# Optimization experiments

Measured on AMD Instinct MI355X. Metric: run time of the kernel, lower is better.

Reference implementation:

```python
import jax, jax.numpy as jnp
import numpy as np

# Config (matches init_kwargs): num_ori=0 -> plain ConvNext path, single scale, knn-16 graph.
N, B, G, K = 16384, 8, 2048, 16   # N nodes = B graphs x G nodes, k-NN with self loops
C, BD, WF, L = 128, 128, 4, 4     # hidden, basis_dim, widening_factor, num layers
POLY_IN = 3                        # PolynomialFeatures(degree=2) on [E,1] dist -> [d, d^2, d^3]


def knn_edges(pos):
    # Graphs are contiguous blocks of G nodes (batch = node // G).
    pg = pos.reshape(B, G, 3)
    d2 = jnp.sum((pg[:, :, None, :] - pg[:, None, :, :]) ** 2, axis=-1)  # [B,G,G]
    _, idx = jax.lax.top_k(-d2, K)                                       # [B,G,K] incl. self (loop=True)
    offset = (jnp.arange(B) * G)[:, None, None]
    src = (idx + offset).reshape(-1)            # neighbor (source) node per edge, [E]
    dst = jnp.repeat(jnp.arange(B * G), K)      # center (target) node per edge, [E]
    return src, dst


def layer_norm(h, g, b):
    mu = jnp.mean(h, axis=-1, keepdims=True)
    var = jnp.var(h, axis=-1, keepdims=True)
    return (h - mu) / jnp.sqrt(var + 1e-5) * g + b


def setup_inputs() -> dict:
    key = jax.random.key(0)
    ks = jax.random.split(key, 20)
    s = 0.05
    inp = {
        'x': jax.random.normal(ks[0], (N, 65), jnp.float32),
        'pos': jax.random.normal(ks[1], (N, 3), jnp.float32),
        'batch': jnp.repeat(jnp.arange(B, dtype=jnp.int32), G),
        # x_embedder (no bias)
        'W_embed': jax.random.normal(ks[2], (65, C), jnp.float32) * s,
        # spatial basis MLP: poly(3) -> Linear -> GELU -> Linear -> GELU
        'Wb1': jax.random.normal(ks[3], (POLY_IN, BD), jnp.float32) * s,
        'bb1': jnp.zeros((BD,), jnp.float32),
        'Wb2': jax.random.normal(ks[4], (BD, BD), jnp.float32) * s,
        'bb2': jnp.zeros((BD,), jnp.float32),
        # per-layer ConvNext params (stacked over L layers)
        'Wk': jax.random.normal(ks[5], (L, BD, C), jnp.float32) * s,  # depthwise conv kernel gen
        'ln_g': jnp.ones((L, C), jnp.float32),
        'ln_b': jnp.zeros((L, C), jnp.float32),
        'W1': jax.random.normal(ks[6], (L, C, WF * C), jnp.float32) * s,
        'b1': jnp.zeros((L, WF * C), jnp.float32),
        'W2': jax.random.normal(ks[7], (L, WF * C, C), jnp.float32) * s,
        'b2': jnp.zeros((L, C), jnp.float32),
        # readout
        'Wr': jax.random.normal(ks[8], (C, 1), jnp.float32) * s,
        'br': jnp.zeros((1,), jnp.float32),
    }
    return inp


def reference(x, pos, batch, W_embed, Wb1, bb1, Wb2, bb2, Wk, ln_g, ln_b, W1, b1, W2, b2, Wr, br):
    src, dst = knn_edges(pos)
    # SEn invariant with num_ori=0: pairwise distance (eps for self-loop grad safety)
    diff = pos[src] - pos[dst]                                    # [E,3]
    d = jnp.sqrt(jnp.sum(diff * diff, axis=-1, keepdims=True) + 1e-12)  # [E,1]
    # PolynomialFeatures(degree=2): [d, d^2, d^3]
    poly = jnp.concatenate([d, d * d, d * d * d], axis=-1)        # [E,3]
    kb = jax.nn.gelu(poly @ Wb1 + bb1)
    kernel = jax.nn.gelu(kb @ Wb2 + bb2)                          # [E,BD] spatial kernel basis

    h = x @ W_embed                                               # [N,C]
    for i in range(L):
        # depthwise conv: per-edge kernel from basis, gather-multiply-scatter
        k_i = kernel @ Wk[i]                                      # [E,C]
        msg = h[src] * k_i                                        # [E,C]
        agg = jax.ops.segment_sum(msg, dst, num_segments=N)       # [N,C]
        z = layer_norm(agg, ln_g[i], ln_b[i])
        z = jax.nn.gelu(z @ W1[i] + b1[i]) @ W2[i] + b2[i]        # pointwise inverted-bottleneck
        h = h + z                                                 # residual (in==out channels)
    out = h @ Wr + br                                             # readout, [N,1] scalar output
    return out
```

## Files before the change

### kernel.cpp

```cpp
#include <hip/hip_runtime.h>
#include <hip/hip_bf16.h>

#define NN 16384
#define GG 2048
#define KNN 16
#define EE (NN*KNN)
#define NL 4

typedef _Float16 f16;
typedef _Float16 half8 __attribute__((ext_vector_type(8)));
typedef _Float16 half4 __attribute__((ext_vector_type(4)));
typedef float f32x4 __attribute__((ext_vector_type(4)));
typedef unsigned long long u64;

__device__ __forceinline__ float gelu_tanh(float x) {
  float s = x*x;
  float u = __fmaf_rn(-0.0713548194f, s, -1.5957691216f);
  float p = __expf(x*u);
  return x * __builtin_amdgcn_rcpf(1.0f + p);
}

__device__ __forceinline__ int mbcnt64(u64 m) {
  return __builtin_amdgcn_mbcnt_hi((unsigned)(m >> 32),
         __builtin_amdgcn_mbcnt_lo((unsigned)m, 0));
}

__global__ __launch_bounds__(256) void knn_kernel(const float* __restrict__ pos,
    int* __restrict__ srci, float* __restrict__ dedge) {
  __shared__ u64 sel[4][16];
  int tid = threadIdx.x;
  int wv = tid >> 6;
  int node = blockIdx.x*4 + wv;
  int lane = tid & 63;
  int base = node & ~(GG-1);
  float qx = pos[(size_t)node*3+0], qy = pos[(size_t)node*3+1], qz = pos[(size_t)node*3+2];

  float d2s[32];
  float c0 = 3.4e38f, c1 = 3.4e38f, c2 = 3.4e38f, c3 = 3.4e38f;
  #pragma unroll
  for (int it = 0; it < 32; ++it) {
    int j = it*64 + lane;
    const float* pr = pos + (size_t)(base+j)*3;
    float dx = __fsub_rn(qx, pr[0]);
    float dy = __fsub_rn(qy, pr[1]);
    float dz = __fsub_rn(qz, pr[2]);
    float d2 = __fadd_rn(__fadd_rn(__fmul_rn(dx,dx), __fmul_rn(dy,dy)), __fmul_rn(dz,dz));
    d2s[it] = d2;
    float x = d2;
    float t0 = fminf(c0, x); x = fmaxf(c0, x); c0 = t0;
    float t1 = fminf(c1, x); x = fmaxf(c1, x); c1 = t1;
    float t2 = fminf(c2, x); x = fmaxf(c2, x); c2 = t2;
    c3 = fminf(c3, x);
  }
  unsigned T = 0;
  for (int b = 30; b >= 0; --b) {
    unsigned tb = T | (1u << b);
    float tf = __uint_as_float(tb);
    int cnt = __popcll(__ballot(c0 < tf)) + __popcll(__ballot(c1 < tf))
            + __popcll(__ballot(c2 < tf)) + __popcll(__ballot(c3 < tf));
    if (cnt < 16) T = tb;
  }
  float Tf = __uint_as_float(T);
  int cless;
  if (!__any(c3 <= Tf)) {
    cless = __popcll(__ballot(c0 < Tf)) + __popcll(__ballot(c1 < Tf))
          + __popcll(__ballot(c2 < Tf)) + __popcll(__ballot(c3 < Tf));
  } else {
    T = 0;
    for (int b = 30; b >= 0; --b) {
      unsigned tb = T | (1u << b);
      float tf = __uint_as_float(tb);
      int cnt = 0;
      #pragma unroll
      for (int q = 0; q < 32; ++q) cnt += __popcll(__ballot(d2s[q] < tf));
      if (cnt < 16) T = tb;
    }
    Tf = __uint_as_float(T);
    cless = 0;
    #pragma unroll
    for (int q = 0; q < 32; ++q) cless += __popcll(__ballot(d2s[q] < Tf));
  }
  int offb = 0;
  int tieq = 16 - cless;
  #pragma unroll
  for (int it = 0; it < 32; ++it) {
    u64 mless = __ballot(d2s[it] < Tf);
    u64 mtie  = __ballot(d2s[it] == Tf);
    bool store = (d2s[it] < Tf);
    int slot = offb + mbcnt64(mless);
    offb += (int)__popcll(mless);
    if (mtie != 0 && tieq > 0) {
      int tr = mbcnt64(mtie);
      if (d2s[it] == Tf && tr < tieq) { store = true; slot = offb + tr; }
      int take = (int)__popcll(mtie); take = take < tieq ? take : tieq;
      offb += take; tieq -= take;
    }
    if (store)
      sel[wv][slot] = ((u64)__float_as_uint(d2s[it]) << 32) | (unsigned)(it*64 + lane);
  }
  if (lane < KNN) {
    u64 e = sel[wv][lane];
    int rank = 0;
    #pragma unroll
    for (int k2 = 0; k2 < 16; ++k2) rank += (sel[wv][k2] < e) ? 1 : 0;
    int j = (int)(e & 0xffffffffu);
    float d2v = __uint_as_float((unsigned)(e >> 32));
    srci[node*KNN + rank] = base + j;
    dedge[node*KNN + rank] = sqrtf(__fadd_rn(d2v, 1e-12f));
  }
}

__global__ __launch_bounds__(256) void prep_kernel(
    const float* __restrict__ Wb2, const float* __restrict__ Wk,
    const float* __restrict__ W1, const float* __restrict__ W2,
    f16* __restrict__ Wb2t, f16* __restrict__ Wkt,
    f16* __restrict__ W1t, f16* __restrict__ W2t) {
  int i = blockIdx.x*256 + threadIdx.x;
  if (i < 16384) {
    int c = i >> 7, k = i & 127;
    Wb2t[i] = (f16)Wb2[k*128 + c];
    return;
  }
  i -= 16384;
  if (i < 65536) {
    int l = i >> 14, r = i & 16383; int c = r >> 7, k = r & 127;
    Wkt[i] = (f16)Wk[l*16384 + k*128 + c];
    return;
  }
  i -= 65536;
  if (i < 262144) {
    int l = i >> 16, r = i & 65535; int c = r >> 7, k = r & 127;
    W1t[i] = (f16)W1[l*65536 + k*512 + c];
    return;
  }
  i -= 262144;
  if (i < 262144) {
    int l = i >> 16, r = i & 65535; int c = r >> 9, k = r & 511;
    W2t[i] = (f16)W2[l*65536 + k*128 + c];
  }
}

__global__ __launch_bounds__(256) void embed_kernel(const float* __restrict__ x,
    const float* __restrict__ We, float* __restrict__ h) {
  int t = threadIdx.x;
  int n = blockIdx.x*8 + (t >> 5);
  int q = (t & 31) * 4;
  f32x4 acc = {0.f,0.f,0.f,0.f};
  const float* xr = x + n*65;
  for (int k = 0; k < 65; ++k) {
    float xv = xr[k];
    f32x4 wv = *(const f32x4*)(We + k*128 + q);
    acc += xv * wv;
  }
  *(f32x4*)(h + (size_t)n*128 + q) = acc;
}

__global__ __launch_bounds__(256) void basis_kernel(const float* __restrict__ dedge,
    const float* __restrict__ Wb1, const float* __restrict__ bb1,
    const f16* __restrict__ Wb2t, const float* __restrict__ bb2,
    f16* __restrict__ kernA) {
  __shared__ f16 Wb2s[128][136];
  __shared__ f16 kb[64][136];
  int t = threadIdx.x;
  #pragma unroll
  for (int it = 0; it < 8; ++it) {
    int idx = it*256 + t;
    int row = idx >> 4, k8 = (idx & 15) * 8;
    *(half8*)&Wb2s[row][k8] = *(const half8*)&Wb2t[row*128 + k8];
  }
  __syncthreads();
  int w = t >> 6, l = t & 63;
  int row4 = l >> 4, rlo = l & 15;
  #pragma unroll
  for (int tt = 0; tt < 2; ++tt) {
    size_t Tg = (size_t)blockIdx.x*8 + (size_t)w*2 + tt;
    float d = dedge[Tg*16 + rlo];
    float d2 = d*d, d3 = d2*d;
    half8 a[4];
    #pragma unroll
    for (int kc = 0; kc < 4; ++kc) {
      int k0 = kc*32 + row4*8;
      f32x4 w1a = *(const f32x4*)&Wb1[k0],     w1b = *(const f32x4*)&Wb1[k0+4];
      f32x4 w2a = *(const f32x4*)&Wb1[128+k0], w2b = *(const f32x4*)&Wb1[128+k0+4];
      f32x4 w3a = *(const f32x4*)&Wb1[256+k0], w3b = *(const f32x4*)&Wb1[256+k0+4];
      f32x4 bba = *(const f32x4*)&bb1[k0],     bbb = *(const f32x4*)&bb1[k0+4];
      #pragma unroll
      for (int j = 0; j < 4; ++j) {
        a[kc][j]   = (f16)gelu_tanh(d*w1a[j] + d2*w2a[j] + d3*w3a[j] + bba[j]);
        a[kc][4+j] = (f16)gelu_tanh(d*w1b[j] + d2*w2b[j] + d3*w3b[j] + bbb[j]);
      }
    }
    f32x4 acc[8];
    #pragma unroll
    for (int nt = 0; nt < 8; ++nt) {
      acc[nt] = (f32x4){0.f,0.f,0.f,0.f};
      #pragma unroll
      for (int kc = 0; kc < 4; ++kc) {
        half8 b = *(const half8*)&Wb2s[nt*16 + rlo][kc*32 + row4*8];
        acc[nt] = __builtin_amdgcn_mfma_f32_16x16x32_f16(a[kc], b, acc[nt], 0, 0, 0);
      }
    }
    #pragma unroll
    for (int nt = 0; nt < 8; ++nt) {
      float bias = bb2[nt*16 + rlo];
      #pragma unroll
      for (int j = 0; j < 4; ++j)
        kb[w*16 + row4*4 + j][nt*16 + rlo] = (f16)gelu_tanh(acc[nt][j] + bias);
    }
    #pragma unroll
    for (int kc = 0; kc < 4; ++kc) {
      half8 v = *(const half8*)&kb[w*16 + rlo][kc*32 + row4*8];
      *(half8*)&kernA[((Tg*4 + kc)*64 + l)*8] = v;
    }
  }
}

#define LOADA(arr, mm) { \
  int node_ = n0 + w*4 + (mm); \
  _Pragma("unroll") \
  for (int kc = 0; kc < 4; ++kc) \
    arr[kc] = *(const half8*)&kernA[(((size_t)node_*4 + kc)*64 + l)*8]; }

#define COMPM(arr, mm) { \
  float hv[4][4]; \
  _Pragma("unroll") \
  for (int nt4 = 0; nt4 < 4; ++nt4) \
    _Pragma("unroll") \
    for (int j = 0; j < 4; ++j) \
      hv[nt4][j] = hin[(size_t)sidxA[mm][j]*128 + (hh*4 + nt4)*16 + rlo]; \
  _Pragma("unroll") \
  for (int nt4 = 0; nt4 < 4; ++nt4) { \
    f32x4 acc = {0.f,0.f,0.f,0.f}; \
    _Pragma("unroll") \
    for (int kc = 0; kc < 4; ++kc) \
      acc = __builtin_amdgcn_mfma_f32_16x16x32_f16(arr[kc], bf[nt4][kc], acc, 0, 0, 0); \
    float p = 0.f; \
    _Pragma("unroll") \
    for (int j = 0; j < 4; ++j) p += acc[j] * hv[nt4][j]; \
    p += __shfl_xor(p, 16, 64); \
    p += __shfl_xor(p, 32, 64); \
    if (l < 16) aggl[w*4 + (mm)][(hh*4 + nt4)*16 + l] = p; \
  } }

__global__ __launch_bounds__(256) void layer_kernel(const f16* __restrict__ kernA,
    const f16* __restrict__ Wkt_l, const int* __restrict__ srci,
    const float* __restrict__ hin,
    const float* __restrict__ lng, const float* __restrict__ lnb,
    const f16* __restrict__ W1t_l, const float* __restrict__ b1_l,
    const f16* __restrict__ W2t_l, const float* __restrict__ b2_l,
    float* __restrict__ hout) {
  __shared__ float aggl[16][132];
  __shared__ f16 zl[16][136];
  __shared__ f16 y1[16][520];
  int t = threadIdx.x;
  int w = t >> 6, l = t & 63;
  int row4 = l >> 4, rlo = l & 15;
  int n0 = blockIdx.x * 16;

  int sidxA[4][4];
  #pragma unroll
  for (int m = 0; m < 4; ++m)
    #pragma unroll
    for (int j = 0; j < 4; ++j)
      sidxA[m][j] = srci[(n0 + w*4 + m)*16 + row4*4 + j];

  #pragma unroll
  for (int hh = 0; hh < 2; ++hh) {
    half8 bf[4][4];
    #pragma unroll
    for (int nt4 = 0; nt4 < 4; ++nt4)
      #pragma unroll
      for (int kc = 0; kc < 4; ++kc)
        bf[nt4][kc] = *(const half8*)&Wkt_l[((hh*4 + nt4)*16 + rlo)*128 + kc*32 + row4*8];
    half8 aA[4], aB[4];
    LOADA(aA, 0)
    LOADA(aB, 1)
    COMPM(aA, 0)
    LOADA(aA, 2)
    COMPM(aB, 1)
    LOADA(aB, 3)
    COMPM(aA, 2)
    COMPM(aB, 3)
  }
  __syncthreads();
  {
    int row = w*4 + row4;
    int cb = rlo*8;
    f32x4 va = *(const f32x4*)&aggl[row][cb];
    f32x4 vb = *(const f32x4*)&aggl[row][cb+4];
    float s = va[0]+va[1]+va[2]+va[3] + vb[0]+vb[1]+vb[2]+vb[3];
    #pragma unroll
    for (int st = 1; st < 16; st <<= 1) s += __shfl_xor(s, st, 64);
    float mu = s * (1.f/128.f);
    f32x4 da = va - mu, db = vb - mu;
    float s2 = da[0]*da[0]+da[1]*da[1]+da[2]*da[2]+da[3]*da[3]
             + db[0]*db[0]+db[1]*db[1]+db[2]*db[2]+db[3]*db[3];
    #pragma unroll
    for (int st = 1; st < 16; st <<= 1) s2 += __shfl_xor(s2, st, 64);
    float inv = rsqrtf(s2*(1.f/128.f) + 1e-5f);
    f32x4 ga = *(const f32x4*)&lng[cb], gb = *(const f32x4*)&lng[cb+4];
    f32x4 ba = *(const f32x4*)&lnb[cb], bb = *(const f32x4*)&lnb[cb+4];
    f32x4 za = da*inv*ga + ba, zb = db*inv*gb + bb;
    half8 hz = { (f16)za[0],(f16)za[1],(f16)za[2],(f16)za[3],
                 (f16)zb[0],(f16)zb[1],(f16)zb[2],(f16)zb[3] };
    *(half8*)&zl[row][cb] = hz;
  }
  __syncthreads();
  half8 az[4];
  #pragma unroll
  for (int kc = 0; kc < 4; ++kc)
    az[kc] = *(const half8*)&zl[rlo][kc*32 + row4*8];
  #pragma unroll
  for (int ntl = 0; ntl < 8; ++ntl) {
    int nt = w*8 + ntl;
    int col = nt*16 + rlo;
    f32x4 acc = {0.f,0.f,0.f,0.f};
    #pragma unroll
    for (int kc = 0; kc < 4; ++kc) {
      half8 b = *(const half8*)&W1t_l[(size_t)col*128 + kc*32 + row4*8];
      acc = __builtin_amdgcn_mfma_f32_16x16x32_f16(az[kc], b, acc, 0, 0, 0);
    }
    float bias = b1_l[col];
    #pragma unroll
    for (int j = 0; j < 4; ++j)
      y1[row4*4 + j][col] = (f16)gelu_tanh(acc[j] + bias);
  }
  __syncthreads();
  half8 a2[16];
  #pragma unroll
  for (int kc2 = 0; kc2 < 16; ++kc2)
    a2[kc2] = *(const half8*)&y1[rlo][kc2*32 + row4*8];
  f32x4 acc2[2] = {{0.f,0.f,0.f,0.f},{0.f,0.f,0.f,0.f}};
  #pragma unroll
  for (int nt2 = 0; nt2 < 2; ++nt2) {
    int c = (w*2 + nt2)*16 + rlo;
    #pragma unroll
    for (int kc2 = 0; kc2 < 16; ++kc2) {
      half8 b = *(const half8*)&W2t_l[(size_t)c*512 + kc2*32 + row4*8];
      acc2[nt2] = __builtin_amdgcn_mfma_f32_16x16x32_f16(a2[kc2], b, acc2[nt2], 0, 0, 0);
    }
  }
  #pragma unroll
  for (int nt2 = 0; nt2 < 2; ++nt2) {
    int col = (w*2 + nt2)*16 + rlo;
    float bias = b2_l[col];
    #pragma unroll
    for (int j = 0; j < 4; ++j) {
      size_t n = (size_t)(n0 + row4*4 + j);
      hout[n*128 + col] = acc2[nt2][j] + bias + hin[n*128 + col];
    }
  }
}

__global__ __launch_bounds__(256) void readout_kernel(const float* __restrict__ h,
    const float* __restrict__ Wr, const float* __restrict__ br, float* __restrict__ out) {
  int n = blockIdx.x*256 + threadIdx.x;
  f32x4 acc = {0.f,0.f,0.f,0.f};
  #pragma unroll
  for (int cb = 0; cb < 32; ++cb) {
    f32x4 hv = *(const f32x4*)(h + (size_t)n*128 + cb*4);
    f32x4 wv = *(const f32x4*)(Wr + cb*4);
    acc += hv*wv;
  }
  out[n] = acc[0]+acc[1]+acc[2]+acc[3] + br[0];
}

extern "C" void kernel_launch(void* const* d_in, const int* in_sizes, int n_in,
                              void* d_out, int out_size, void* d_ws, size_t ws_size,
                              hipStream_t stream) {
  const float* x   = (const float*)d_in[0];
  const float* pos = (const float*)d_in[1];
  const float* We  = (const float*)d_in[3];
  const float* Wb1 = (const float*)d_in[4];
  const float* bb1 = (const float*)d_in[5];
  const float* Wb2 = (const float*)d_in[6];
  const float* bb2 = (const float*)d_in[7];
  const float* Wk  = (const float*)d_in[8];
  const float* lng = (const float*)d_in[9];
  const float* lnb = (const float*)d_in[10];
  const float* W1  = (const float*)d_in[11];
  const float* b1  = (const float*)d_in[12];
  const float* W2  = (const float*)d_in[13];
  const float* b2  = (const float*)d_in[14];
  const float* Wr  = (const float*)d_in[15];
  const float* br  = (const float*)d_in[16];
  float* out = (float*)d_out;

  char* p = (char*)d_ws;
  int*   srci  = (int*)p;     p += (size_t)EE*4;
  float* dedge = (float*)p;   p += (size_t)EE*4;
  f16*   kernA = (f16*)p;     p += (size_t)EE*128*2;
  float* hA    = (float*)p;   p += (size_t)NN*128*4;
  float* hB    = (float*)p;   p += (size_t)NN*128*4;
  f16* Wb2t    = (f16*)p;     p += (size_t)16384*2;
  f16* Wkt     = (f16*)p;     p += (size_t)65536*2;
  f16* W1t     = (f16*)p;     p += (size_t)262144*2;
  f16* W2t     = (f16*)p;     p += (size_t)262144*2;

  prep_kernel<<<2368, 256, 0, stream>>>(Wb2, Wk, W1, W2, Wb2t, Wkt, W1t, W2t);
  knn_kernel<<<NN/4, 256, 0, stream>>>(pos, srci, dedge);
  basis_kernel<<<2048, 256, 0, stream>>>(dedge, Wb1, bb1, Wb2t, bb2, kernA);
  embed_kernel<<<NN/8, 256, 0, stream>>>(x, We, hA);
  float* hin = hA;
  for (int lyr = 0; lyr < NL; ++lyr) {
    float* hout = (hin == hA) ? hB : hA;
    layer_kernel<<<NN/16, 256, 0, stream>>>(kernA, Wkt + lyr*16384, srci, hin,
        lng + lyr*128, lnb + lyr*128,
        W1t + (size_t)lyr*65536, b1 + lyr*512, W2t + (size_t)lyr*65536, b2 + lyr*128, hout);
    hin = hout;
  }
  readout_kernel<<<NN/256, 256, 0, stream>>>(hin, Wr, br, out);
}
```

Before: 353.9 us.

## Prefetch neighbor features, remap block order, and cap occupancy in layer kernel

Splits the gather of neighbor h values from the compute macro so each node's hin loads are issued together with its kernel-basis loads, one node ahead of the MFMA work, to hide gather latency. It also permutes block indices so consecutive blocks work on nodes spread across graphs, probably to spread L2/channel traffic, and adds a min-blocks-per-CU hint to launch_bounds. The prefetch raises register pressure. It also leaves an empty dead loop at the end of the kernel.

```diff
diff --git a/kernel.cpp b/kernel.cpp
--- a/kernel.cpp
+++ b/kernel.cpp
@@ -221,13 +221,14 @@
   for (int kc = 0; kc < 4; ++kc) \
     arr[kc] = *(const half8*)&kernA[(((size_t)node_*4 + kc)*64 + l)*8]; }
 
-#define COMPM(arr, mm) { \
-  float hv[4][4]; \
+#define PREH(hvv, mm) { \
   _Pragma("unroll") \
   for (int nt4 = 0; nt4 < 4; ++nt4) \
     _Pragma("unroll") \
     for (int j = 0; j < 4; ++j) \
-      hv[nt4][j] = hin[(size_t)sidxA[mm][j]*128 + (hh*4 + nt4)*16 + rlo]; \
+      hvv[nt4][j] = hin[(size_t)sidxA[mm][j]*128 + (hh*4 + nt4)*16 + rlo]; }
+
+#define COMPU(arr, hvv, mm) { \
   _Pragma("unroll") \
   for (int nt4 = 0; nt4 < 4; ++nt4) { \
     f32x4 acc = {0.f,0.f,0.f,0.f}; \
@@ -236,13 +237,13 @@
       acc = __builtin_amdgcn_mfma_f32_16x16x32_f16(arr[kc], bf[nt4][kc], acc, 0, 0, 0); \
     float p = 0.f; \
     _Pragma("unroll") \
-    for (int j = 0; j < 4; ++j) p += acc[j] * hv[nt4][j]; \
+    for (int j = 0; j < 4; ++j) p += acc[j] * hvv[nt4][j]; \
     p += __shfl_xor(p, 16, 64); \
     p += __shfl_xor(p, 32, 64); \
     if (l < 16) aggl[w*4 + (mm)][(hh*4 + nt4)*16 + l] = p; \
   } }
 
-__global__ __launch_bounds__(256) void layer_kernel(const f16* __restrict__ kernA,
+__global__ __launch_bounds__(256, 4) void layer_kernel(const f16* __restrict__ kernA,
     const f16* __restrict__ Wkt_l, const int* __restrict__ srci,
     const float* __restrict__ hin,
     const float* __restrict__ lng, const float* __restrict__ lnb,
@@ -255,7 +256,8 @@
   int t = threadIdx.x;
   int w = t >> 6, l = t & 63;
   int row4 = l >> 4, rlo = l & 15;
-  int n0 = blockIdx.x * 16;
+  int bid = (blockIdx.x & 7)*128 + (blockIdx.x >> 3);
+  int n0 = bid * 16;
 
   int sidxA[4][4];
   #pragma unroll
@@ -273,14 +275,15 @@
       for (int kc = 0; kc < 4; ++kc)
         bf[nt4][kc] = *(const half8*)&Wkt_l[((hh*4 + nt4)*16 + rlo)*128 + kc*32 + row4*8];
     half8 aA[4], aB[4];
-    LOADA(aA, 0)
-    LOADA(aB, 1)
-    COMPM(aA, 0)
-    LOADA(aA, 2)
-    COMPM(aB, 1)
-    LOADA(aB, 3)
-    COMPM(aA, 2)
-    COMPM(aB, 3)
+    float vA[4][4], vB[4][4];
+    LOADA(aA, 0) PREH(vA, 0)
+    LOADA(aB, 1) PREH(vB, 1)
+    COMPU(aA, vA, 0)
+    LOADA(aA, 2) PREH(vA, 2)
+    COMPU(aB, vB, 1)
+    LOADA(aB, 3) PREH(vB, 3)
+    COMPU(aA, vA, 2)
+    COMPU(aB, vB, 3)
   }
   __syncthreads();
   {
@@ -338,6 +341,15 @@
     for (int kc2 = 0; kc2 < 16; ++kc2) {
       half8 b = *(const half8*)&W2t_l[(size_t)c*512 + kc2*32 + row4*8];
       acc2[nt2] = __builtin_amdgcn_mfma_f32_16x16x32_f16(a2[kc2], b, acc2[nt2], 0, 0, 0);
+    }
+  }
+  #pragma unroll
+  for (int nt2 = 0; nt2 < 2; ++nt2) {
+    int col = (w*2 + nt2)*16 + rlo;
+    float bias = b2_l[col];
+    #pragma unroll
+    for (int j = 0; j < 4; ++j) {
+      size_t n = (size_t)(n0 + w*4 + 0) ;
     }
   }
   #pragma unroll
```

Result: slower. 554.4 us (+56.7%).
